# Kernel optimization log

Hardware: AMD Instinct MI355X
Metric: run time of the kernel (lower is better)

## Reference

```python
import math
import jax, jax.numpy as jnp
import numpy as np

DIMS = 20
MULT = 8
K = (DIMS + 1) * MULT  # 168 mixture components
N = 524288
EPS = 1.0              # log_density default eps
BASE_COV = 0.1
LOG_NORM = -DIMS / 2 * math.log(2 * math.pi)


def setup_inputs() -> dict:
    key = jax.random.key(0)
    k1, k2, k3 = jax.random.split(key, 3)
    sample = jax.random.normal(k1, (N, DIMS), dtype=jnp.float32) * 0.3
    alpha = jax.random.normal(k2, (K,), dtype=jnp.float32) * 0.1
    mu = jax.random.uniform(k3, (K, DIMS), dtype=jnp.float32, minval=-0.5, maxval=0.5)
    cov = jnp.full((K, DIMS), BASE_COV, dtype=jnp.float32)
    return {"sample": sample, "alpha": alpha, "mu": mu, "cov": cov}


def reference(sample, alpha, mu, cov):
    # Faithful vectorization of the per-component Python loop in log_density.
    var = EPS ** 2
    weights = jax.nn.softmax(alpha)                       # [K]
    i = jnp.arange(K) // MULT                             # component group index, 0..DIMS
    d = jnp.arange(DIMS)
    # cov[:i] *= var  ->  scale first i dims of each component's cov by var
    scale = jnp.where(d[None, :] < i[:, None], var, 1.0)  # [K, D]
    inv = 1.0 / (cov * scale)                             # [K, D]
    # det_cov = var**i * (1/10)**(dims - i)  (exactly as in the source)
    fi = i.astype(jnp.float32)
    det_cov = var ** fi * BASE_COV ** (DIMS - fi)         # [K]
    sig_term = det_cov ** -0.5                            # [K]
    # quad[n,k] = sum_d (x[n,d]-mu[k,d])^2 * inv[k,d], expanded into GEMMs
    quad = (sample ** 2) @ inv.T \
           - 2.0 * (sample @ (mu * inv).T) \
           + jnp.sum(mu * mu * inv, axis=1)[None, :]      # [N, K]
    results = sig_term * jnp.exp(-0.5 * quad) * weights   # [N, K]
    density = results.sum(axis=1, keepdims=True)          # [N, 1]
    return jnp.log(density) + LOG_NORM
```

## Files before the change

### kernel.cpp

```cpp
#include <hip/hip_runtime.h>
#include <math.h>


#define DIMS     20
#define MULT     8
#define K_COMP   168
#define KC_PAD   176
#define BROW     72
#define BASE_COV 0.1f
#define LOG2E    1.4426950408889634f
#define LN2      0.6931471805599453f
#define LOG_NORM -18.378770664093453f
#define CPW      8
#define NB       1024

typedef _Float16 f16x8 __attribute__((ext_vector_type(8)));
typedef _Float16 f16x2 __attribute__((ext_vector_type(2)));
typedef float    f32x4 __attribute__((ext_vector_type(4)));
typedef unsigned int uint;
typedef uint u32x4 __attribute__((ext_vector_type(4)));

__device__ __forceinline__ uint pk(float lo, float hi) {
    return __builtin_bit_cast(uint, __builtin_amdgcn_cvt_pkrtz(lo, hi));
}
__device__ __forceinline__ uint pksq(uint a) {
    f16x2 v = __builtin_bit_cast(f16x2, a);
    return __builtin_bit_cast(uint, (f16x2)(v * v));
}

__global__ __launch_bounds__(256, 3) void gm_fused(const float* __restrict__ sample,
                                                   const float* __restrict__ alpha,
                                                   const float* __restrict__ mu,
                                                   const float* __restrict__ cov,
                                                   float* __restrict__ out) {
    __shared__ __attribute__((aligned(16))) _Float16 lds_T[KC_PAD][BROW];
    __shared__ float sh_logZ;
    const int tid = threadIdx.x;

    uint* bz = (uint*)&lds_T[0][0];
    for (int i = tid; i < KC_PAD * BROW / 2; i += 256) bz[i] = 0u;
    __syncthreads();

    if (tid < 64) {
        float a0 = (tid       < K_COMP) ? alpha[tid]       : -1e30f;
        float a1 = (tid + 64  < K_COMP) ? alpha[tid + 64]  : -1e30f;
        float a2 = (tid + 128 < K_COMP) ? alpha[tid + 128] : -1e30f;
        float m = fmaxf(fmaxf(a0, a1), a2);
        for (int msk = 32; msk; msk >>= 1) m = fmaxf(m, __shfl_xor(m, msk, 64));
        float s = __expf(a0 - m) + __expf(a1 - m) + __expf(a2 - m);
        for (int msk = 32; msk; msk >>= 1) s += __shfl_xor(s, msk, 64);
        if (tid == 0) sh_logZ = m + __logf(s);
    }
    __syncthreads();

    if (tid < K_COMP) {
        const int   n  = tid;
        const int   i  = n / MULT;
        const float fi = (float)i;
        const float var = 1.0f;
        float logdet = fi * __logf(var) + ((float)DIMS - fi) * __logf(BASE_COV);
        const float4* cvp = (const float4*)(cov + n * DIMS);
        const float4* mup = (const float4*)(mu + n * DIMS);
        float4 c0 = cvp[0], c1 = cvp[1], c2 = cvp[2], c3 = cvp[3], c4 = cvp[4];
        float4 m0 = mup[0], m1 = mup[1], m2 = mup[2], m3 = mup[3], m4 = mup[4];
        float C = 0.0f;
        auto emit = [&](int d, float cc, float mm) {
            float scale = (d < i) ? var : 1.0f;
            float inv   = 1.0f / (cc * scale);
            C += mm * mm * inv;
            lds_T[n][d]        = (_Float16)(-0.5f * inv * LOG2E);
            lds_T[n][DIMS + d] = (_Float16)(mm * inv * LOG2E);
        };
        emit( 0, c0.x, m0.x); emit( 1, c0.y, m0.y); emit( 2, c0.z, m0.z); emit( 3, c0.w, m0.w);
        emit( 4, c1.x, m1.x); emit( 5, c1.y, m1.y); emit( 6, c1.z, m1.z); emit( 7, c1.w, m1.w);
        emit( 8, c2.x, m2.x); emit( 9, c2.y, m2.y); emit(10, c2.z, m2.z); emit(11, c2.w, m2.w);
        emit(12, c3.x, m3.x); emit(13, c3.y, m3.y); emit(14, c3.z, m3.z); emit(15, c3.w, m3.w);
        emit(16, c4.x, m4.x); emit(17, c4.y, m4.y); emit(18, c4.z, m4.z); emit(19, c4.w, m4.w);
        float L2 = ((alpha[n] - sh_logZ) - 0.5f * logdet - 0.5f * C) * LOG2E;
        lds_T[n][2 * DIMS] = (_Float16)L2;
    } else if (tid < KC_PAD) {
        lds_T[tid][2 * DIMS] = (_Float16)(-65504.0f);
    }
    __syncthreads();

    const int w = tid >> 6, l = tid & 63, q = l >> 4, c = l & 15;
    const bool qa = (q & 1) != 0, qb = (q & 2) != 0;
    const uint onezero = 0x00003C00u;
    const f32x4 zero = { 0.f, 0.f, 0.f, 0.f };

#define LOAD_CF(T)                                                              \
    const f16x8 cf1_##T = *(const f16x8*)&lds_T[(T) * 16 + c][q * 8];           \
    const f16x8 cf2_##T = *(const f16x8*)&lds_T[(T) * 16 + c][32 + q * 8];
    LOAD_CF(0) LOAD_CF(1) LOAD_CF(2) LOAD_CF(3) LOAD_CF(4) LOAD_CF(5)
    LOAD_CF(6) LOAD_CF(7) LOAD_CF(8) LOAD_CF(9) LOAD_CF(10)
#undef LOAD_CF

    const int base = blockIdx.x * (64 * CPW) + w * 16;

    const float4* rp0 = (const float4*)(sample + (size_t)(base + c) * DIMS);
    float4 r0 = rp0[0], r1 = rp0[1], r2 = rp0[2], r3 = rp0[3], r4 = rp0[4];

#define DO_TILE(T)                                                              \
        {                                                                       \
            f32x4 acc = __builtin_amdgcn_mfma_f32_16x16x32_f16(cf1_##T, sf1, zero, 0, 0, 0); \
            acc       = __builtin_amdgcn_mfma_f32_16x16x32_f16(cf2_##T, sf2, acc,  0, 0, 0); \
            p0 += __builtin_amdgcn_exp2f(acc[0]);                               \
            p1 += __builtin_amdgcn_exp2f(acc[1]);                               \
            p2 += __builtin_amdgcn_exp2f(acc[2]);                               \
            p3 += __builtin_amdgcn_exp2f(acc[3]);                               \
        }

#define DO_CHUNK(CC)                                                            \
    {                                                                           \
                                      \
        uint q0 = pk(r0.x, r0.y), q1 = pk(r0.z, r0.w);                          \
        uint q2 = pk(r1.x, r1.y), q3 = pk(r1.z, r1.w);                          \
        uint q4 = pk(r2.x, r2.y), q5 = pk(r2.z, r2.w);                          \
        uint q6 = pk(r3.x, r3.y), q7 = pk(r3.z, r3.w);                          \
        uint q8 = pk(r4.x, r4.y), q9 = pk(r4.z, r4.w);                          \
         \
         \
         \
         \
        if ((CC) + 1 < CPW) {                                                   \
            uint dep = q9;                                                      \
            asm volatile("v_and_b32 %0, 0, %0" : "+v"(dep));                    \
            const float4* np = (const float4*)(sample                           \
                + (size_t)(base + ((CC) + 1) * 64 + c) * DIMS + dep);           \
            r0 = np[0]; r1 = np[1]; r2 = np[2]; r3 = np[3]; r4 = np[4];         \
        }                                                                       \
        uint s0 = pksq(q0), s1 = pksq(q1), s2 = pksq(q2), s3 = pksq(q3);        \
        uint s4 = pksq(q4), s5 = pksq(q5), s6 = pksq(q6), s7 = pksq(q7);        \
        uint s8 = pksq(q8), s9 = pksq(q9);                                      \
        uint f1_0 = qb ? (qa ? q2 : s8) : (qa ? s4 : s0);                       \
        uint f1_1 = qb ? (qa ? q3 : s9) : (qa ? s5 : s1);                       \
        uint f1_2 = qb ? (qa ? q4 : q0) : (qa ? s6 : s2);                       \
        uint f1_3 = qb ? (qa ? q5 : q1) : (qa ? s7 : s3);                       \
        uint f2_0 = qb ? 0u : (qa ? onezero : q6);                              \
        uint f2_1 = qb ? 0u : (qa ? 0u : q7);                                   \
        uint f2_2 = qb ? 0u : (qa ? 0u : q8);                                   \
        uint f2_3 = qb ? 0u : (qa ? 0u : q9);                                   \
        u32x4 w1 = { f1_0, f1_1, f1_2, f1_3 };                                  \
        u32x4 w2 = { f2_0, f2_1, f2_2, f2_3 };                                  \
        f16x8 sf1 = __builtin_bit_cast(f16x8, w1);                              \
        f16x8 sf2 = __builtin_bit_cast(f16x8, w2);                              \
        float p0 = 0.f, p1 = 0.f, p2 = 0.f, p3 = 0.f;       \
        DO_TILE(0) DO_TILE(1) DO_TILE(2) DO_TILE(3) DO_TILE(4) DO_TILE(5)       \
        DO_TILE(6) DO_TILE(7) DO_TILE(8) DO_TILE(9) DO_TILE(10)                 \
        float dens = (p0 + p1) + (p2 + p3);                                     \
        dens += __shfl_xor(dens, 16, 64);                                       \
        dens += __shfl_xor(dens, 32, 64);                                       \
        if (l < 16)                                                             \
            out[base + (CC) * 64 + l] = LN2 * __builtin_amdgcn_logf(dens) + LOG_NORM; \
    }

    DO_CHUNK(0) DO_CHUNK(1) DO_CHUNK(2) DO_CHUNK(3)
    DO_CHUNK(4) DO_CHUNK(5) DO_CHUNK(6) DO_CHUNK(7)
#undef DO_CHUNK
#undef DO_TILE
}

extern "C" void kernel_launch(void* const* d_in, const int* in_sizes, int n_in,
                              void* d_out, int out_size, void* d_ws, size_t ws_size,
                              hipStream_t stream) {
    const float* sample = (const float*)d_in[0];
    const float* alpha  = (const float*)d_in[1];
    const float* mu     = (const float*)d_in[2];
    const float* cov    = (const float*)d_in[3];
    float* out = (float*)d_out;
    gm_fused<<<NB, 256, 0, stream>>>(sample, alpha, mu, cov, out);
}
```

Measured before the change: 97.57 us.

## Split coefficient precompute into separate kernel and stream table from global

Moves the per-component coefficient table construction (softmax, inverse covariances, fp16 packing) out of every block into a single-block precompute kernel that writes a lane-ordered MFMA fragment table to workspace. The density kernel becomes a 64-thread block with 4 chunks of 16 samples each, loading its fragments directly from global/L2 instead of rebuilding LDS per block. This removes redundant per-block setup and LDS/barriers, but adds a second launch with a serial single-block dependency and many more, smaller blocks.

New measurement: 97.06 us. No clear change (-0.5%).

```diff
diff --git a/kernel.cpp b/kernel.cpp
--- a/kernel.cpp
+++ b/kernel.cpp
@@ -6,13 +6,13 @@
 #define MULT     8
 #define K_COMP   168
 #define KC_PAD   176
-#define BROW     72
+#define NTILE    11
 #define BASE_COV 0.1f
 #define LOG2E    1.4426950408889634f
 #define LN2      0.6931471805599453f
 #define LOG_NORM -18.378770664093453f
-#define CPW      8
-#define NB       1024
+#define CPW      4
+#define NBLK     8192
 
 typedef _Float16 f16x8 __attribute__((ext_vector_type(8)));
 typedef _Float16 f16x2 __attribute__((ext_vector_type(2)));
@@ -28,17 +28,16 @@
     return __builtin_bit_cast(uint, (f16x2)(v * v));
 }
 
-__global__ __launch_bounds__(256, 3) void gm_fused(const float* __restrict__ sample,
-                                                   const float* __restrict__ alpha,
-                                                   const float* __restrict__ mu,
-                                                   const float* __restrict__ cov,
-                                                   float* __restrict__ out) {
-    __shared__ __attribute__((aligned(16))) _Float16 lds_T[KC_PAD][BROW];
+__global__ void gm_precompute(const float* __restrict__ alpha,
+                              const float* __restrict__ mu,
+                              const float* __restrict__ cov,
+                              uint4* __restrict__ tbl) {
+    __shared__ _Float16 C[KC_PAD][64];
     __shared__ float sh_logZ;
     const int tid = threadIdx.x;
 
-    uint* bz = (uint*)&lds_T[0][0];
-    for (int i = tid; i < KC_PAD * BROW / 2; i += 256) bz[i] = 0u;
+    uint* cz = (uint*)&C[0][0];
+    for (int i = tid; i < KC_PAD * 64 / 2; i += 256) cz[i] = 0u;
     __syncthreads();
 
     if (tid < 64) {
@@ -59,43 +58,48 @@
         const float fi = (float)i;
         const float var = 1.0f;
         float logdet = fi * __logf(var) + ((float)DIMS - fi) * __logf(BASE_COV);
-        const float4* cvp = (const float4*)(cov + n * DIMS);
-        const float4* mup = (const float4*)(mu + n * DIMS);
-        float4 c0 = cvp[0], c1 = cvp[1], c2 = cvp[2], c3 = cvp[3], c4 = cvp[4];
-        float4 m0 = mup[0], m1 = mup[1], m2 = mup[2], m3 = mup[3], m4 = mup[4];
-        float C = 0.0f;
-        auto emit = [&](int d, float cc, float mm) {
+        float Csum = 0.0f;
+        for (int d = 0; d < DIMS; ++d) {
             float scale = (d < i) ? var : 1.0f;
-            float inv   = 1.0f / (cc * scale);
-            C += mm * mm * inv;
-            lds_T[n][d]        = (_Float16)(-0.5f * inv * LOG2E);
-            lds_T[n][DIMS + d] = (_Float16)(mm * inv * LOG2E);
-        };
-        emit( 0, c0.x, m0.x); emit( 1, c0.y, m0.y); emit( 2, c0.z, m0.z); emit( 3, c0.w, m0.w);
-        emit( 4, c1.x, m1.x); emit( 5, c1.y, m1.y); emit( 6, c1.z, m1.z); emit( 7, c1.w, m1.w);
-        emit( 8, c2.x, m2.x); emit( 9, c2.y, m2.y); emit(10, c2.z, m2.z); emit(11, c2.w, m2.w);
-        emit(12, c3.x, m3.x); emit(13, c3.y, m3.y); emit(14, c3.z, m3.z); emit(15, c3.w, m3.w);
-        emit(16, c4.x, m4.x); emit(17, c4.y, m4.y); emit(18, c4.z, m4.z); emit(19, c4.w, m4.w);
-        float L2 = ((alpha[n] - sh_logZ) - 0.5f * logdet - 0.5f * C) * LOG2E;
-        lds_T[n][2 * DIMS] = (_Float16)L2;
+            float inv   = 1.0f / (cov[n * DIMS + d] * scale);
+            float mm    = mu[n * DIMS + d];
+            Csum += mm * mm * inv;
+            C[n][d]        = (_Float16)(-0.5f * inv * LOG2E);
+            C[n][DIMS + d] = (_Float16)(mm * inv * LOG2E);
+        }
+        float L2 = ((alpha[n] - sh_logZ) - 0.5f * logdet - 0.5f * Csum) * LOG2E;
+        C[n][2 * DIMS] = (_Float16)L2;
     } else if (tid < KC_PAD) {
-        lds_T[tid][2 * DIMS] = (_Float16)(-65504.0f);
+        C[tid][2 * DIMS] = (_Float16)(-65504.0f);
     }
     __syncthreads();
 
-    const int w = tid >> 6, l = tid & 63, q = l >> 4, c = l & 15;
+    for (int e = tid; e < NTILE * 2 * 64; e += 256) {
+        int t    = e >> 7;
+        int h    = (e >> 6) & 1;
+        int lane = e & 63;
+        int q = lane >> 4, c = lane & 15;
+        tbl[e] = *(const uint4*)&C[t * 16 + c][h * 32 + q * 8];
+    }
+}
+
+__global__ __launch_bounds__(64, 3) void gm_density(const float* __restrict__ sample,
+                                                    const f16x8* __restrict__ tbl,
+                                                    float* __restrict__ out) {
+    const int l = threadIdx.x;
+    const int q = l >> 4, c = l & 15;
     const bool qa = (q & 1) != 0, qb = (q & 2) != 0;
     const uint onezero = 0x00003C00u;
     const f32x4 zero = { 0.f, 0.f, 0.f, 0.f };
 
 #define LOAD_CF(T)                                                              \
-    const f16x8 cf1_##T = *(const f16x8*)&lds_T[(T) * 16 + c][q * 8];           \
-    const f16x8 cf2_##T = *(const f16x8*)&lds_T[(T) * 16 + c][32 + q * 8];
+    const f16x8 cf1_##T = tbl[(T) * 128 + l];                                   \
+    const f16x8 cf2_##T = tbl[(T) * 128 + 64 + l];
     LOAD_CF(0) LOAD_CF(1) LOAD_CF(2) LOAD_CF(3) LOAD_CF(4) LOAD_CF(5)
     LOAD_CF(6) LOAD_CF(7) LOAD_CF(8) LOAD_CF(9) LOAD_CF(10)
 #undef LOAD_CF
 
-    const int base = blockIdx.x * (64 * CPW) + w * 16;
+    const int base = blockIdx.x * (16 * CPW);
 
     const float4* rp0 = (const float4*)(sample + (size_t)(base + c) * DIMS);
     float4 r0 = rp0[0], r1 = rp0[1], r2 = rp0[2], r3 = rp0[3], r4 = rp0[4];
@@ -112,7 +116,6 @@
 
 #define DO_CHUNK(CC)                                                            \
     {                                                                           \
-                                      \
         uint q0 = pk(r0.x, r0.y), q1 = pk(r0.z, r0.w);                          \
         uint q2 = pk(r1.x, r1.y), q3 = pk(r1.z, r1.w);                          \
         uint q4 = pk(r2.x, r2.y), q5 = pk(r2.z, r2.w);                          \
@@ -120,13 +123,11 @@
         uint q8 = pk(r4.x, r4.y), q9 = pk(r4.z, r4.w);                          \
          \
          \
-         \
-         \
         if ((CC) + 1 < CPW) {                                                   \
             uint dep = q9;                                                      \
             asm volatile("v_and_b32 %0, 0, %0" : "+v"(dep));                    \
             const float4* np = (const float4*)(sample                           \
-                + (size_t)(base + ((CC) + 1) * 64 + c) * DIMS + dep);           \
+                + (size_t)(base + ((CC) + 1) * 16 + c) * DIMS + dep);           \
             r0 = np[0]; r1 = np[1]; r2 = np[2]; r3 = np[3]; r4 = np[4];         \
         }                                                                       \
         uint s0 = pksq(q0), s1 = pksq(q1), s2 = pksq(q2), s3 = pksq(q3);        \
@@ -151,11 +152,10 @@
         dens += __shfl_xor(dens, 16, 64);                                       \
         dens += __shfl_xor(dens, 32, 64);                                       \
         if (l < 16)                                                             \
-            out[base + (CC) * 64 + l] = LN2 * __builtin_amdgcn_logf(dens) + LOG_NORM; \
+            out[base + (CC) * 16 + l] = LN2 * __builtin_amdgcn_logf(dens) + LOG_NORM; \
     }
 
     DO_CHUNK(0) DO_CHUNK(1) DO_CHUNK(2) DO_CHUNK(3)
-    DO_CHUNK(4) DO_CHUNK(5) DO_CHUNK(6) DO_CHUNK(7)
 #undef DO_CHUNK
 #undef DO_TILE
 }
@@ -168,5 +168,8 @@
     const float* mu     = (const float*)d_in[2];
     const float* cov    = (const float*)d_in[3];
     float* out = (float*)d_out;
-    gm_fused<<<NB, 256, 0, stream>>>(sample, alpha, mu, cov, out);
+    uint4* tbl = (uint4*)d_ws;
+
+    gm_precompute<<<1, 256, 0, stream>>>(alpha, mu, cov, tbl);
+    gm_density<<<NBLK, 64, 0, stream>>>(sample, (const f16x8*)tbl, out);
 }
```
